# Kernel optimization log

Hardware: AMD Instinct MI355X
Metric: run time of the kernel (lower is better)

## Reference

```python
import jax, jax.numpy as jnp
import numpy as np

N_NODES = 50000
N_EDGES = 800000
NFEAT, NHID, NCLASS = 256, 128, 32
MAX_DEG = 48  # safe upper bound on in-degree: mean 16 (+1 self loop), Poisson tail << 48


def _median_conv(x, src, dst, W, b, max_deg=MAX_DEG):
    """MedianConv: h = x @ W; remove self loops; add one self loop per node;
    per-destination median aggregation (lower median, like torch.median); + bias."""
    N, F = x.shape[0], W.shape[1]
    h = x @ W  # [N, F]
    # torch: remove_self_loops then add_self_loops -> effective edges are all
    # non-self edges plus exactly one self loop per node. Route original self
    # loops into a trash segment (index N) to keep shapes static.
    dst_eff = jnp.where(src == dst, N, dst)
    ar = jnp.arange(N)
    src_all = jnp.concatenate([src, ar])          # [E+N]
    dst_all = jnp.concatenate([dst_eff, ar])      # [E+N]
    E = src_all.shape[0]
    order = jnp.argsort(dst_all)                  # group edges by destination
    d_s = dst_all[order]
    msg = h[src_all[order]]                       # [E+N, F] gathered messages
    deg = jax.ops.segment_sum(jnp.ones(E, jnp.int32), d_s, num_segments=N + 1)
    offsets = jnp.cumsum(deg) - deg               # start of each segment
    pos = jnp.arange(E) - offsets[d_s]            # slot within segment
    # dense batch padded with +inf so padding sorts to the end
    dense = jnp.full((N + 1, max_deg, F), jnp.inf, h.dtype)
    dense = dense.at[d_s, pos].set(msg)
    dense = jnp.sort(dense, axis=1)               # per-feature sort within segment
    med_idx = (deg[:N] - 1) // 2                  # lower median (torch.median)
    out = jnp.take_along_axis(dense[:N], med_idx[:, None, None], axis=1)[:, 0, :]
    return out + b


def setup_inputs() -> dict:
    key = jax.random.key(0)
    k1, k2, k3, k4, k5, k6 = jax.random.split(key, 6)
    features = jax.random.normal(k1, (N_NODES, NFEAT), dtype=jnp.float32)
    edge_index = jax.random.randint(k2, (2, N_EDGES), 0, N_NODES, dtype=jnp.int64)
    # Linear weights stored as [in, out] (transpose of torch layout)
    W1 = jax.random.normal(k3, (NFEAT, NHID), dtype=jnp.float32) * 0.05
    b1 = jnp.zeros((NHID,), dtype=jnp.float32)
    W2 = jax.random.normal(k4, (NHID, NCLASS), dtype=jnp.float32) * 0.05
    b2 = jnp.zeros((NCLASS,), dtype=jnp.float32)
    return {"features": features, "edge_index": edge_index,
            "W1": W1, "b1": b1, "W2": W2, "b2": b2}


def reference(features, edge_index, W1, b1, W2, b2):
    src, dst = edge_index[0], edge_index[1]
    # dropout is identity in eval mode
    x = _median_conv(features, src, dst, W1, b1)
    x = jax.nn.relu(x)
    x = _median_conv(x, src, dst, W2, b2)
    return jax.nn.log_softmax(x, axis=1)
```

## Files before the change

### kernel.cpp

```cpp
#include <hip/hip_runtime.h>
#include <hip/hip_bf16.h>
#include <math.h>

#define N_NODES 50000
#define N_EDGES 800000
#define NFEAT 256
#define NHID 128
#define NCLASS 32
#define STRIDE 48
#define G1B 782

#define NBKT 196
#define CAPB 6144
#define TILE 2048
#define NTILE ((N_EDGES + TILE - 1) / TILE)

#define INFF __builtin_inff()

typedef unsigned short ushort_t;
typedef unsigned int uint_t;
typedef __bf16 bf16x8 __attribute__((ext_vector_type(8)));
typedef float f32x4 __attribute__((ext_vector_type(4)));
typedef unsigned short u16x2 __attribute__((ext_vector_type(2)));

__device__ __forceinline__ float bf2f(ushort_t u) {
  union { unsigned int i; float f; } c;
  c.i = ((unsigned int)u) << 16;
  return c.f;
}
__device__ __forceinline__ ushort_t f2bf(float f) {
  unsigned int x = __float_as_uint(f);
  unsigned int r = (x + 0x7fff + ((x >> 16) & 1)) >> 16;
  return (ushort_t)r;
}
__device__ __forceinline__ ushort_t bf2sort(ushort_t b) {
  return b ^ ((b & 0x8000) ? 0xFFFFu : 0x8000u);
}
__device__ __forceinline__ ushort_t sort2bf(ushort_t s) {
  return s ^ ((s & 0x8000) ? 0x8000u : 0xFFFFu);
}


__global__ __launch_bounds__(256) void pre_k(const float* __restrict__ X,
                                             const float* __restrict__ W,
                                             ushort_t* __restrict__ H1,
                                             const int* __restrict__ src,
                                             const int* __restrict__ dst,
                                             int* __restrict__ gcnt,
                                             uint_t* __restrict__ buf) {
  __shared__ __attribute__((aligned(16))) char smem[15360];
  int bid = blockIdx.x;
  int tid = threadIdx.x;

  if (bid >= G1B) {
    uint_t* val = reinterpret_cast<uint_t*>(smem);
    int* scanbuf = reinterpret_cast<int*>(smem + 8192);
    int* hist = reinterpret_cast<int*>(smem + 9216);
    int* lbase = reinterpret_cast<int*>(smem + 10000);
    int* gbase = reinterpret_cast<int*>(smem + 10784);
    int* lcur = reinterpret_cast<int*>(smem + 11568);
    unsigned char* bkt = reinterpret_cast<unsigned char*>(smem + 12352);

    int e0 = (bid - G1B) * TILE;
    for (int b = tid; b < NBKT; b += 256) hist[b] = 0;
    __syncthreads();

    int myb[TILE / 256];
    uint_t myv[TILE / 256];
#pragma unroll
    for (int j = 0; j < TILE / 256; ++j) {
      int i = e0 + j * 256 + tid;
      int b = -1;
      uint_t v = 0;
      if (i < N_EDGES) {
        int s = src[i], d = dst[i];
        if (s != d) {
          b = d >> 8;
          v = ((uint_t)(d & 255) << 16) | (uint_t)s;
          atomicAdd(&hist[b], 1);
        }
      }
      myb[j] = b;
      myv[j] = v;
    }
    __syncthreads();

    if (tid < NBKT) gbase[tid] = atomicAdd(&gcnt[tid], hist[tid]);
    scanbuf[tid] = (tid < NBKT) ? hist[tid] : 0;
    __syncthreads();
    for (int off = 1; off < 256; off <<= 1) {
      int v = (tid >= off) ? scanbuf[tid - off] : 0;
      __syncthreads();
      scanbuf[tid] += v;
      __syncthreads();
    }
    if (tid < NBKT) {
      lbase[tid] = scanbuf[tid] - hist[tid];
      lcur[tid] = 0;
    }
    __syncthreads();

#pragma unroll
    for (int j = 0; j < TILE / 256; ++j) {
      int b = myb[j];
      if (b >= 0) {
        int sl = lbase[b] + atomicAdd(&lcur[b], 1);
        val[sl] = myv[j];
        bkt[sl] = (unsigned char)b;
      }
    }
    __syncthreads();

    int ntot = scanbuf[255];
    for (int sl = tid; sl < ntot; sl += 256) {
      int b = bkt[sl];
      int off = gbase[b] + (sl - lbase[b]);
      if (off < CAPB) buf[(size_t)b * CAPB + off] = val[sl];
    }
    return;
  }

  ushort_t (*As)[40] = reinterpret_cast<ushort_t(*)[40]>(smem);
  ushort_t (*Bs)[40] = reinterpret_cast<ushort_t(*)[40]>(smem + 5120);

  int rb = bid * 64;
  int lane = tid & 63, wid = tid >> 6;
  int wm = wid >> 1, wn = wid & 1;
  int lrow = lane & 15, lk = (lane >> 4) * 8;
  int arow = tid >> 2, akq = (tid & 3) * 8;
  int bn = tid & 127, bkh = tid >> 7;

  f32x4 acc[2][4];
#pragma unroll
  for (int m = 0; m < 2; ++m)
#pragma unroll
    for (int n = 0; n < 4; ++n) acc[m][n] = (f32x4){0.f, 0.f, 0.f, 0.f};

  for (int kc = 0; kc < NFEAT; kc += 32) {
    {
      int grow = rb + arow;
      bf16x8 p;
      if (grow < N_NODES) {
        const float* gp = X + (size_t)grow * NFEAT + kc + akq;
        float4 v0 = *reinterpret_cast<const float4*>(gp);
        float4 v1 = *reinterpret_cast<const float4*>(gp + 4);
        p[0] = (__bf16)v0.x; p[1] = (__bf16)v0.y; p[2] = (__bf16)v0.z; p[3] = (__bf16)v0.w;
        p[4] = (__bf16)v1.x; p[5] = (__bf16)v1.y; p[6] = (__bf16)v1.z; p[7] = (__bf16)v1.w;
      } else {
        p = (bf16x8)(__bf16)0.f;
      }
      *reinterpret_cast<bf16x8*>(&As[arow][akq]) = p;
    }
    {
      const float* gp = W + (size_t)(kc + bkh * 16) * NHID + bn;
      bf16x8 p0, p1;
#pragma unroll
      for (int j = 0; j < 8; ++j) p0[j] = (__bf16)gp[(size_t)j * NHID];
#pragma unroll
      for (int j = 0; j < 8; ++j) p1[j] = (__bf16)gp[(size_t)(8 + j) * NHID];
      *reinterpret_cast<bf16x8*>(&Bs[bn][bkh * 16]) = p0;
      *reinterpret_cast<bf16x8*>(&Bs[bn][bkh * 16 + 8]) = p1;
    }
    __syncthreads();
    bf16x8 af[2], bfr[4];
#pragma unroll
    for (int m = 0; m < 2; ++m)
      af[m] = *reinterpret_cast<const bf16x8*>(&As[wm * 32 + m * 16 + lrow][lk]);
#pragma unroll
    for (int n = 0; n < 4; ++n)
      bfr[n] = *reinterpret_cast<const bf16x8*>(&Bs[wn * 64 + n * 16 + lrow][lk]);
#pragma unroll
    for (int m = 0; m < 2; ++m)
#pragma unroll
      for (int n = 0; n < 4; ++n)
        acc[m][n] = __builtin_amdgcn_mfma_f32_16x16x32_bf16(af[m], bfr[n], acc[m][n], 0, 0, 0);
    __syncthreads();
  }
#pragma unroll
  for (int m = 0; m < 2; ++m) {
    int row0 = rb + wm * 32 + m * 16 + (lane >> 4) * 4;
#pragma unroll
    for (int n = 0; n < 4; ++n) {
      int col = wn * 64 + n * 16 + lrow;
#pragma unroll
      for (int j = 0; j < 4; ++j) {
        int r = row0 + j;
        if (r < N_NODES) H1[(size_t)r * NHID + col] = bf2sort(f2bf(acc[m][n][j]));
      }
    }
  }
}


__global__ __launch_bounds__(256) void build_k(const int* __restrict__ gcnt,
                                               const uint_t* __restrict__ buf,
                                               int* __restrict__ cur,
                                               ushort_t* __restrict__ adjw) {
  __shared__ __attribute__((aligned(16))) ushort_t rows[256 * STRIDE];
  __shared__ int cnt[256];
  int b = blockIdx.x, tid = threadIdx.x;
  int v0 = b << 8;
  int nv = N_NODES - v0;
  if (nv > 256) nv = 256;
  cnt[tid] = 1;
  if (tid < nv) rows[tid * STRIDE] = (ushort_t)(v0 + tid);
  __syncthreads();

  int n = gcnt[b];
  if (n > CAPB) n = CAPB;
  for (int i = tid; i < n; i += 256) {
    uint_t e = buf[(size_t)b * CAPB + i];
    int s = e & 0xFFFF;
    int doff = e >> 16;
    int p = atomicAdd(&cnt[doff], 1);
    if (p < STRIDE) rows[doff * STRIDE + p] = (ushort_t)s;
  }
  __syncthreads();

  int nq = nv * 6;
  uint4* gout = reinterpret_cast<uint4*>(adjw + (size_t)v0 * STRIDE);
  const uint4* ls = reinterpret_cast<const uint4*>(rows);
  for (int i = tid; i < nq; i += 256) gout[i] = ls[i];
  if (tid < nv) cur[v0 + tid] = cnt[tid] - 1;
}


__global__ __launch_bounds__(256) void gemm2_k(const uint_t* __restrict__ X1u,
                                               const float* __restrict__ W,
                                               ushort_t* __restrict__ H2s) {
  __shared__ ushort_t As[128][136];
  __shared__ ushort_t Bs[32][136];
  int tid = threadIdx.x;
  int rb = blockIdx.x * 128;
  int lane = tid & 63, wid = tid >> 6;
  int lrow = lane & 15, lk = (lane >> 4) * 8;

#pragma unroll
  for (int j = 0; j < 8; ++j) {
    int f = tid + j * 256;
    int row = f >> 4;
    int q = f & 15;
    int grow = rb + row;
    uint4 v = make_uint4(0, 0, 0, 0);
    if (grow < N_NODES)
      v = *reinterpret_cast<const uint4*>(X1u + (size_t)grow * 64 + q * 4);
    *reinterpret_cast<uint4*>(&As[row][q * 8]) = v;
  }
  {
    int bn = tid & 31, bq = tid >> 5;
    const float* gp = W + (size_t)(bq * 16) * NCLASS + bn;
    bf16x8 p0, p1;
#pragma unroll
    for (int j = 0; j < 8; ++j) p0[j] = (__bf16)gp[(size_t)j * NCLASS];
#pragma unroll
    for (int j = 0; j < 8; ++j) p1[j] = (__bf16)gp[(size_t)(8 + j) * NCLASS];
    *reinterpret_cast<bf16x8*>(&Bs[bn][bq * 16]) = p0;
    *reinterpret_cast<bf16x8*>(&Bs[bn][bq * 16 + 8]) = p1;
  }
  __syncthreads();

  f32x4 acc[2][2];
#pragma unroll
  for (int m = 0; m < 2; ++m)
#pragma unroll
    for (int n = 0; n < 2; ++n) acc[m][n] = (f32x4){0.f, 0.f, 0.f, 0.f};

#pragma unroll
  for (int ks = 0; ks < 4; ++ks) {
    bf16x8 af[2], bfr[2];
#pragma unroll
    for (int m = 0; m < 2; ++m)
      af[m] = *reinterpret_cast<const bf16x8*>(&As[wid * 32 + m * 16 + lrow][ks * 32 + lk]);
#pragma unroll
    for (int n = 0; n < 2; ++n)
      bfr[n] = *reinterpret_cast<const bf16x8*>(&Bs[n * 16 + lrow][ks * 32 + lk]);
#pragma unroll
    for (int m = 0; m < 2; ++m)
#pragma unroll
      for (int n = 0; n < 2; ++n)
        acc[m][n] = __builtin_amdgcn_mfma_f32_16x16x32_bf16(af[m], bfr[n], acc[m][n], 0, 0, 0);
  }
#pragma unroll
  for (int m = 0; m < 2; ++m) {
    int row0 = rb + wid * 32 + m * 16 + (lane >> 4) * 4;
#pragma unroll
    for (int n = 0; n < 2; ++n) {
      int col = n * 16 + lrow;
#pragma unroll
      for (int j = 0; j < 4; ++j) {
        int r = row0 + j;
        if (r < N_NODES) H2s[(size_t)r * NCLASS + col] = bf2sort(f2bf(acc[m][n][j]));
      }
    }
  }
}


template <int NP>
__device__ __forceinline__ void pk_sort(u16x2 (&a)[NP]) {
#pragma unroll
  for (int p = 1; p < NP; p <<= 1) {
#pragma unroll
    for (int q = p; q >= 1; q >>= 1) {
#pragma unroll
      for (int j = q % p; j + q < NP; j += 2 * q) {
#pragma unroll
        for (int i = 0; i < q; ++i) {
          int lo = i + j, hi = i + j + q;
          if (hi < NP && (lo / (2 * p)) == (hi / (2 * p))) {
            u16x2 x = a[lo], y = a[hi];
            a[lo] = __builtin_elementwise_min(x, y);
            a[hi] = __builtin_elementwise_max(x, y);
          }
        }
      }
    }
  }
}


template <int KP>
__device__ __forceinline__ uint_t med1_path(const uint_t* __restrict__ H1p, int sreg,
                                            int k, int m, int t) {
  u16x2 a[KP];
#pragma unroll
  for (int e = 0; e < KP; ++e) {
    uint_t pu = 0xFFFFFFFFu;
    if (e < k) {
      int s = __builtin_amdgcn_readlane(sreg, e);
      pu = H1p[(size_t)s * 64 + t];
    }
    union { uint_t u; u16x2 v; } c;
    c.u = pu;
    a[e] = c.v;
  }
  pk_sort<KP>(a);
  u16x2 med = a[0];
#pragma unroll
  for (int i = 1; i <= (KP - 1) / 2; ++i)
    if (i == m) med = a[i];
  union { u16x2 v; uint_t u; } r;
  r.v = med;
  return r.u;
}

__global__ __launch_bounds__(256, 8) void med1_k(const ushort_t* __restrict__ H1,
                                                 const int* __restrict__ cur,
                                                 const ushort_t* __restrict__ adjw,
                                                 const float* __restrict__ b1,
                                                 uint_t* __restrict__ X1u) {
  int v = blockIdx.x * 4 + (threadIdx.x >> 6);
  int t = threadIdx.x & 63;
  int k = cur[v] + 1;
  if (k > STRIDE) k = STRIDE;
  k = __builtin_amdgcn_readfirstlane(k);
  int sreg = adjw[v * STRIDE + ((t < k) ? t : 0)];
  int m = (k - 1) >> 1;
  const uint_t* H1p = reinterpret_cast<const uint_t*>(H1);
  uint_t mu;
  if (k <= 16)      mu = med1_path<16>(H1p, sreg, k, m, t);
  else if (k <= 20) mu = med1_path<20>(H1p, sreg, k, m, t);
  else if (k <= 24) mu = med1_path<24>(H1p, sreg, k, m, t);
  else if (k <= 28) mu = med1_path<28>(H1p, sreg, k, m, t);
  else if (k <= 32) mu = med1_path<32>(H1p, sreg, k, m, t);
  else              mu = med1_path<48>(H1p, sreg, k, m, t);
  ushort_t s0 = (ushort_t)(mu & 0xFFFF), s1 = (ushort_t)(mu >> 16);
  float2 bb = *reinterpret_cast<const float2*>(b1 + 2 * t);
  float f0 = fmaxf(bf2f(sort2bf(s0)) + bb.x, 0.f);
  float f1 = fmaxf(bf2f(sort2bf(s1)) + bb.y, 0.f);
  X1u[(size_t)v * 64 + t] = (uint_t)f2bf(f0) | ((uint_t)f2bf(f1) << 16);
}


template <int KP>
__device__ __forceinline__ uint_t med2_path(const uint_t* __restrict__ H2p,
                                            int s0, int s1, int s2,
                                            int k, int m, int g, int l) {
  u16x2 a[KP];
#pragma unroll
  for (int e = 0; e < KP; ++e) {
    int sr = (e < 16) ? s0 : ((e < 32) ? s1 : s2);
    int srcid = __shfl(sr, g * 16 + (e & 15), 64);
    uint_t u = H2p[(size_t)srcid * 16 + l];
    uint_t pu = (e < k) ? u : 0xFFFFFFFFu;
    union { uint_t u; u16x2 v; } c;
    c.u = pu;
    a[e] = c.v;
  }
  pk_sort<KP>(a);
  u16x2 med = a[0];
#pragma unroll
  for (int i = 1; i <= (KP - 1) / 2; ++i)
    if (i == m) med = a[i];
  union { u16x2 v; uint_t u; } r;
  r.v = med;
  return r.u;
}

__global__ __launch_bounds__(256, 8) void med2_k(const ushort_t* __restrict__ H2,
                                                 const int* __restrict__ cur,
                                                 const ushort_t* __restrict__ adjw,
                                                 const float* __restrict__ b2,
                                                 float* __restrict__ OUT) {
  int w = threadIdx.x >> 6;
  int t = threadIdx.x & 63;
  int l = t & 15, g = t >> 4;
  int vh = (blockIdx.x * 4 + w) * 4 + g;
  int k = cur[vh] + 1;
  if (k > STRIDE) k = STRIDE;
  int m = (k - 1) >> 1;
  int base = vh * STRIDE;
  int s0 = adjw[base + ((l < k) ? l : 0)];
  int s1 = adjw[base + ((16 + l < k) ? 16 + l : 0)];
  int s2 = adjw[base + ((32 + l < k) ? 32 + l : 0)];
  int kmax = max(k, __shfl_xor(k, 16, 64));
  kmax = max(kmax, __shfl_xor(kmax, 32, 64));
  const uint_t* H2p = reinterpret_cast<const uint_t*>(H2);
  uint_t mu;
  if (kmax <= 16)      mu = med2_path<16>(H2p, s0, s1, s2, k, m, g, l);
  else if (kmax <= 20) mu = med2_path<20>(H2p, s0, s1, s2, k, m, g, l);
  else if (kmax <= 24) mu = med2_path<24>(H2p, s0, s1, s2, k, m, g, l);
  else if (kmax <= 28) mu = med2_path<28>(H2p, s0, s1, s2, k, m, g, l);
  else if (kmax <= 32) mu = med2_path<32>(H2p, s0, s1, s2, k, m, g, l);
  else                 mu = med2_path<48>(H2p, s0, s1, s2, k, m, g, l);
  ushort_t u0 = (ushort_t)(mu & 0xFFFF), u1 = (ushort_t)(mu >> 16);
  float2 bb = *reinterpret_cast<const float2*>(b2 + 2 * l);
  float f0 = bf2f(sort2bf(u0)) + bb.x;
  float f1 = bf2f(sort2bf(u1)) + bb.y;
  float mx = fmaxf(f0, f1);
#pragma unroll
  for (int s = 8; s; s >>= 1) mx = fmaxf(mx, __shfl_xor(mx, s, 16));
  float sum = expf(f0 - mx) + expf(f1 - mx);
#pragma unroll
  for (int s = 8; s; s >>= 1) sum += __shfl_xor(sum, s, 16);
  float lg = logf(sum);
  float2 res = make_float2(f0 - mx - lg, f1 - mx - lg);
  *reinterpret_cast<float2*>(&OUT[(size_t)vh * NCLASS + 2 * l]) = res;
}


extern "C" void kernel_launch(void* const* d_in, const int* in_sizes, int n_in,
                              void* d_out, int out_size, void* d_ws, size_t ws_size,
                              hipStream_t stream) {
  const float* X = (const float*)d_in[0];
  const int* src = (const int*)d_in[1];
  const int* dst = src + N_EDGES;
  const float* W1 = (const float*)d_in[2];
  const float* b1 = (const float*)d_in[3];
  const float* W2 = (const float*)d_in[4];
  const float* b2 = (const float*)d_in[5];
  float* OUT = (float*)d_out;

  char* w = (char*)d_ws;
  size_t o = 0;
  auto take = [&](size_t bytes) {
    void* p = w + o;
    o += (bytes + 255) & ~(size_t)255;
    return p;
  };
  int* cur = (int*)take(N_NODES * sizeof(int));
  ushort_t* adjw = (ushort_t*)take((size_t)N_NODES * STRIDE * sizeof(ushort_t));
  ushort_t* h1 = (ushort_t*)take((size_t)N_NODES * NHID * sizeof(ushort_t));
  uint_t* x1 = (uint_t*)take((size_t)N_NODES * 64 * sizeof(uint_t));
  ushort_t* h2 = (ushort_t*)take((size_t)N_NODES * NCLASS * sizeof(ushort_t));
  int* gcnt = (int*)take(256 * sizeof(int));
  uint_t* buf = (uint_t*)take((size_t)NBKT * CAPB * sizeof(uint_t));
  (void)ws_size;

  hipMemsetAsync(gcnt, 0, 256 * sizeof(int), stream);
  pre_k<<<G1B + NTILE, 256, 0, stream>>>(X, W1, h1, src, dst, gcnt, buf);
  build_k<<<NBKT, 256, 0, stream>>>(gcnt, buf, cur, adjw);
  med1_k<<<N_NODES / 4, 256, 0, stream>>>(h1, cur, adjw, b1, x1);
  gemm2_k<<<(N_NODES + 127) / 128, 256, 0, stream>>>(x1, W2, h2);
  med2_k<<<N_NODES / 16, 256, 0, stream>>>(h2, cur, adjw, b2, OUT);
}
```

Before: 100.5 us.

## Replace global atomic bucket allocation with fixed per-tile slots

```diff
diff --git a/kernel.cpp b/kernel.cpp
--- a/kernel.cpp
+++ b/kernel.cpp
@@ -11,9 +11,9 @@
 #define G1B 782
 
 #define NBKT 196
-#define CAPB 6144
 #define TILE 2048
 #define NTILE ((N_EDGES + TILE - 1) / TILE)
+#define TCAP 40
 
 #define INFF __builtin_inff()
 
@@ -46,7 +46,7 @@
                                              ushort_t* __restrict__ H1,
                                              const int* __restrict__ src,
                                              const int* __restrict__ dst,
-                                             int* __restrict__ gcnt,
+                                             int* __restrict__ tcnt,
                                              uint_t* __restrict__ buf) {
   __shared__ __attribute__((aligned(16))) char smem[15360];
   int bid = blockIdx.x;
@@ -57,11 +57,11 @@
     int* scanbuf = reinterpret_cast<int*>(smem + 8192);
     int* hist = reinterpret_cast<int*>(smem + 9216);
     int* lbase = reinterpret_cast<int*>(smem + 10000);
-    int* gbase = reinterpret_cast<int*>(smem + 10784);
-    int* lcur = reinterpret_cast<int*>(smem + 11568);
-    unsigned char* bkt = reinterpret_cast<unsigned char*>(smem + 12352);
-
-    int e0 = (bid - G1B) * TILE;
+    int* lcur = reinterpret_cast<int*>(smem + 10784);
+    unsigned char* bkt = reinterpret_cast<unsigned char*>(smem + 11568);
+
+    int q = bid - G1B;
+    int e0 = q * TILE;
     for (int b = tid; b < NBKT; b += 256) hist[b] = 0;
     __syncthreads();
 
@@ -85,7 +85,6 @@
     }
     __syncthreads();
 
-    if (tid < NBKT) gbase[tid] = atomicAdd(&gcnt[tid], hist[tid]);
     scanbuf[tid] = (tid < NBKT) ? hist[tid] : 0;
     __syncthreads();
     for (int off = 1; off < 256; off <<= 1) {
@@ -97,6 +96,7 @@
     if (tid < NBKT) {
       lbase[tid] = scanbuf[tid] - hist[tid];
       lcur[tid] = 0;
+      tcnt[q * NBKT + tid] = (hist[tid] < TCAP) ? hist[tid] : TCAP;
     }
     __syncthreads();
 
@@ -114,8 +114,8 @@
     int ntot = scanbuf[255];
     for (int sl = tid; sl < ntot; sl += 256) {
       int b = bkt[sl];
-      int off = gbase[b] + (sl - lbase[b]);
-      if (off < CAPB) buf[(size_t)b * CAPB + off] = val[sl];
+      int off = sl - lbase[b];
+      if (off < TCAP) buf[((size_t)b * NTILE + q) * TCAP + off] = val[sl];
     }
     return;
   }
@@ -192,28 +192,32 @@
 }
 
 
-__global__ __launch_bounds__(256) void build_k(const int* __restrict__ gcnt,
+__global__ __launch_bounds__(256) void build_k(const int* __restrict__ tcnt,
                                                const uint_t* __restrict__ buf,
                                                int* __restrict__ cur,
                                                ushort_t* __restrict__ adjw) {
   __shared__ __attribute__((aligned(16))) ushort_t rows[256 * STRIDE];
   __shared__ int cnt[256];
+  __shared__ ushort_t tcl[NTILE];
   int b = blockIdx.x, tid = threadIdx.x;
   int v0 = b << 8;
   int nv = N_NODES - v0;
   if (nv > 256) nv = 256;
   cnt[tid] = 1;
   if (tid < nv) rows[tid * STRIDE] = (ushort_t)(v0 + tid);
+  for (int i = tid; i < NTILE; i += 256) tcl[i] = (ushort_t)tcnt[i * NBKT + b];
   __syncthreads();
 
-  int n = gcnt[b];
-  if (n > CAPB) n = CAPB;
-  for (int i = tid; i < n; i += 256) {
-    uint_t e = buf[(size_t)b * CAPB + i];
-    int s = e & 0xFFFF;
-    int doff = e >> 16;
-    int p = atomicAdd(&cnt[doff], 1);
-    if (p < STRIDE) rows[doff * STRIDE + p] = (ushort_t)s;
+  const uint_t* bb = buf + (size_t)b * NTILE * TCAP;
+  for (int i = tid; i < NTILE * TCAP; i += 256) {
+    int q = i / TCAP, off = i - q * TCAP;
+    if (off < (int)tcl[q]) {
+      uint_t e = bb[i];
+      int s = e & 0xFFFF;
+      int doff = e >> 16;
+      int p = atomicAdd(&cnt[doff], 1);
+      if (p < STRIDE) rows[doff * STRIDE + p] = (ushort_t)s;
+    }
   }
   __syncthreads();
 
@@ -463,13 +467,12 @@
   ushort_t* h1 = (ushort_t*)take((size_t)N_NODES * NHID * sizeof(ushort_t));
   uint_t* x1 = (uint_t*)take((size_t)N_NODES * 64 * sizeof(uint_t));
   ushort_t* h2 = (ushort_t*)take((size_t)N_NODES * NCLASS * sizeof(ushort_t));
-  int* gcnt = (int*)take(256 * sizeof(int));
-  uint_t* buf = (uint_t*)take((size_t)NBKT * CAPB * sizeof(uint_t));
+  int* tcnt = (int*)take((size_t)NTILE * NBKT * sizeof(int));
+  uint_t* buf = (uint_t*)take((size_t)NBKT * NTILE * TCAP * sizeof(uint_t));
   (void)ws_size;
 
-  hipMemsetAsync(gcnt, 0, 256 * sizeof(int), stream);
-  pre_k<<<G1B + NTILE, 256, 0, stream>>>(X, W1, h1, src, dst, gcnt, buf);
-  build_k<<<NBKT, 256, 0, stream>>>(gcnt, buf, cur, adjw);
+  pre_k<<<G1B + NTILE, 256, 0, stream>>>(X, W1, h1, src, dst, tcnt, buf);
+  build_k<<<NBKT, 256, 0, stream>>>(tcnt, buf, cur, adjw);
   med1_k<<<N_NODES / 4, 256, 0, stream>>>(h1, cur, adjw, b1, x1);
   gemm2_k<<<(N_NODES + 127) / 128, 256, 0, stream>>>(x1, W2, h2);
   med2_k<<<N_NODES / 16, 256, 0, stream>>>(h2, cur, adjw, b2, OUT);
```

Measured after the change: 107.3 us. +6.8%, slower.
